# Kernel tuning notes

Hardware: AMD Instinct MI355X
Metric: run time of the kernel (lower is better)

## Reference

```python
import jax, jax.numpy as jnp
import numpy as np

T, B, D, H = 256, 256, 512, 1024


def setup_inputs() -> dict:
    key = jax.random.key(0)
    ks = jax.random.split(key, 9)
    s = 0.02  # small init scale for numerical sanity
    return {
        "inputs": jax.random.normal(ks[0], (T, B, D), dtype=jnp.float32),
        "Wf": jax.random.normal(ks[1], (D + H, H), dtype=jnp.float32) * s,
        "bf": jax.random.normal(ks[2], (H,), dtype=jnp.float32) * s,
        "Wi": jax.random.normal(ks[3], (D + H, H), dtype=jnp.float32) * s,
        "bi": jax.random.normal(ks[4], (H,), dtype=jnp.float32) * s,
        "Wg": jax.random.normal(ks[5], (D + H, H), dtype=jnp.float32) * s,
        "bg": jax.random.normal(ks[6], (H,), dtype=jnp.float32) * s,
        "Wo": jax.random.normal(ks[7], (D + H, H), dtype=jnp.float32) * s,
        "bo": jax.random.normal(ks[8], (H,), dtype=jnp.float32) * s,
    }


def reference(inputs, Wf, bf, Wi, bi, Wg, bg, Wo, bo):
    hidden_dim = Wf.shape[1]
    batch = inputs.shape[1]
    # Fuse the four gate projections into one [D+H, 4H] GEMM per step.
    W = jnp.concatenate([Wf, Wi, Wg, Wo], axis=1)   # [D+H, 4H]
    b = jnp.concatenate([bf, bi, bg, bo], axis=0)   # [4H]

    h0 = jnp.zeros((batch, hidden_dim), dtype=inputs.dtype)
    c0 = jnp.zeros((batch, hidden_dim), dtype=inputs.dtype)

    def step(carry, x):
        hx, cx = carry
        combined = jnp.concatenate([x, hx], axis=1)  # [B, D+H]
        z = combined @ W + b                          # [B, 4H]
        f, i, g, o = jnp.split(z, 4, axis=1)
        f = jax.nn.sigmoid(f)
        i = jax.nn.sigmoid(i)
        g = jnp.tanh(g)
        o = jax.nn.sigmoid(o)
        cx = f * cx + i * g
        hx = o * jnp.tanh(cx)
        return (hx, cx), hx

    (hx, cx), outputs = jax.lax.scan(step, (h0, c0), inputs)
    return outputs, hx, cx
```

## Files before the change

### kernel.cpp

```cpp
#include <hip/hip_runtime.h>
#include <cstdint>
#include <cstddef>

#define T_STEPS 256
#define BATCH   256
#define DIN     512
#define HID     1024
#define KTOT    1536
#define NOUT    4096
#define BHSZ    ((size_t)BATCH * HID)

typedef __bf16 bf16;
typedef __bf16 bf16x4 __attribute__((ext_vector_type(4)));
typedef __bf16 bf16x8 __attribute__((ext_vector_type(8)));
typedef float  f32x4  __attribute__((ext_vector_type(4)));

__device__ __forceinline__ void store_bf16_sc(bf16* p, bf16 v) {
  unsigned short u = __builtin_bit_cast(unsigned short, v);
  asm volatile("global_store_short %0, %1, off sc0 sc1" :: "v"(p), "v"(u) : "memory");
}

#define VMW_(N) asm volatile("s_waitcnt vmcnt(" #N ")" ::: "memory")
#define VMW(N) do { VMW_(N); __builtin_amdgcn_sched_barrier(0); } while (0)
#define LGKM0() do { asm volatile("s_waitcnt lgkmcnt(0)" ::: "memory"); \
                     __builtin_amdgcn_sched_barrier(0); } while (0)
#define SBAR() __builtin_amdgcn_sched_barrier(0)
#define RAWBAR() do { SBAR(); __builtin_amdgcn_s_barrier(); SBAR(); } while (0)

__device__ __forceinline__ float fexp2(float x) {
  float r; asm("v_exp_f32 %0, %1" : "=v"(r) : "v"(x)); return r;
}
__device__ __forceinline__ float frcp(float x) {
  float r; asm("v_rcp_f32 %0, %1" : "=v"(r) : "v"(x)); return r;
}
__device__ __forceinline__ float fsigmoid(float x) {
  return frcp(1.f + fexp2(-1.44269504f * x));
}
__device__ __forceinline__ float ftanh(float x) {
  return 1.f - 2.f * frcp(1.f + fexp2(2.88539008f * x));
}

__global__ void convert_w_kernel(const float* __restrict__ Wf, const float* __restrict__ Wi,
                                 const float* __restrict__ Wg, const float* __restrict__ Wo,
                                 bf16* __restrict__ Wt) {
  __shared__ float tile[64][17];
  const int k0 = blockIdx.x * 64;
  const int jb = blockIdx.y;
  const int j0 = jb * 16;
  const int t  = threadIdx.x;
  const float* srcs[4] = {Wf, Wi, Wg, Wo};
#pragma unroll
  for (int g = 0; g < 4; ++g) {
    const float* src = srcs[g];
    {
      const int jl = t & 15, kb = t >> 4;
#pragma unroll
      for (int r = 0; r < 4; ++r) {
        const int kl = kb + 16 * r;
        tile[kl][jl] = src[(size_t)(k0 + kl) * HID + (j0 + jl)];
      }
    }
    __syncthreads();
    {
      const int kk = t & 63, jl4 = t >> 6;
#pragma unroll
      for (int r = 0; r < 4; ++r) {
        const int jl = jl4 + 4 * r;
        Wt[(size_t)(jb * 64 + g * 16 + jl) * KTOT + (k0 + kk)] = (bf16)tile[kk][jl];
      }
    }
    __syncthreads();
  }
}

__global__ void convert_x_kernel(const float* __restrict__ X, bf16* __restrict__ xb) {
  const int t = blockIdx.y;
  const int i = blockIdx.x * blockDim.x + threadIdx.x;
  const float4 v = ((const float4*)(X + (size_t)t * BATCH * DIN))[i];
  bf16x4 o;
  o[0] = (bf16)v.x; o[1] = (bf16)v.y; o[2] = (bf16)v.z; o[3] = (bf16)v.w;
  ((bf16x4*)(xb + (size_t)t * BATCH * DIN))[i] = o;
}

__global__ __launch_bounds__(512, 2)
void lstm_v14(const bf16* __restrict__ Bt,
              const bf16* __restrict__ xb,
              bf16* __restrict__ hseq,
              const bf16* __restrict__ zb16,
              float* __restrict__ outF,
              const float* __restrict__ bf_, const float* __restrict__ bi_,
              const float* __restrict__ bg_, const float* __restrict__ bo_,
              unsigned* __restrict__ flags) {
  __shared__ f32x4 redu[8][8][64];

  const int tid = threadIdx.x, lane = tid & 63, wid = tid >> 6;
  const int bid = blockIdx.x;
  const int e8  = bid & 7;
  const int mh   = e8 >> 1;
  const int nblk = ((bid >> 3) << 1) | (e8 & 1);
  const int bn0 = nblk * 64;
  const int fr = lane & 15, fq = lane >> 4;
  const int rowA = mh * 32, rowB = 128 + mh * 32;

  if (tid == 0)
    (void)__hip_atomic_load(flags, __ATOMIC_ACQUIRE, __HIP_MEMORY_SCOPE_AGENT);
  __syncthreads();

  const int j = nblk * 16 + fr;
  const float bfv = bf_[j], biv = bi_[j], bgv = bg_[j], bov = bo_[j];
  float crA = 0.f, crB = 0.f;

  bf16x8 breg[6][4];
#pragma unroll
  for (int s = 0; s < 6; ++s) {
    const int ks = wid + 8 * s;
#pragma unroll
    for (int nf = 0; nf < 4; ++nf)
      breg[s][nf] = *(const bf16x8*)(Bt + (size_t)(bn0 + nf * 16 + fr) * KTOT
                                     + ks * 32 + fq * 8);
  }

  bf16x8 P0[2], P1[2], P2[2], P3[2], Q2[2], Q3[2], Q4[2], Q5[2];

  auto ldx = [&](int t2, int rowbase, int s, bf16x8 (&sl)[2]) {
    const bf16* src = xb + (size_t)t2 * BATCH * DIN + (wid + 8 * s) * 32 + fq * 8;
#pragma unroll
    for (int mf = 0; mf < 2; ++mf)
      sl[mf] = *(const bf16x8*)(src + (size_t)(rowbase + mf * 16 + fr) * DIN);
  };
  auto ldh = [&](int t2, int half, int s, bf16x8 (&sl)[2]) {
    const int c0 = (wid + 8 * s) * 32 - 512;
    const int pp = (c0 >> 4) + (fq >> 1);
    const bf16* base = (t2 == 0)
        ? zb16
        : hseq + ((((size_t)(t2 - 1) * 2 + half) << 8) + mh * 64 + pp) * 512;
    const int coloff = (fq & 1) * 8;
#pragma unroll
    for (int mf = 0; mf < 2; ++mf)
      sl[mf] = *(const bf16x8*)(base + (mf * 16 + fr) * 16 + coloff);
  };

  const int pn8 = 2 * wid + ((lane & 7) >> 1) * 16 + (lane & 1);
  auto pollh = [&](int tprev, int half) {
    const unsigned* f = flags + (((size_t)tprev * 2 + half) << 8) + mh * 64 + pn8;
    const unsigned long long tt0 = __builtin_amdgcn_s_memrealtime();
    for (;;) {
      unsigned v = __hip_atomic_load(f, __ATOMIC_RELAXED,
                                     __HIP_MEMORY_SCOPE_AGENT);
      if (__all(v != 0)) break;
      __builtin_amdgcn_s_sleep(1);
      if (__builtin_amdgcn_s_memrealtime() - tt0 > (1ULL << 22)) break;
    }
    asm volatile("" ::: "memory");
    __builtin_amdgcn_sched_barrier(0);
  };

  auto dump = [&](f32x4 (&acc)[2][4]) {
#pragma unroll
    for (int mf = 0; mf < 2; ++mf)
#pragma unroll
      for (int nf = 0; nf < 4; ++nf)
        redu[wid][mf * 4 + nf][lane] = acc[mf][nf];
  };

  auto finish = [&](int t2, int half, float& cre) {
    const int mf_c = wid >> 2;
    const int lsel = (wid & 3) * 16 + fr;
    float z[4];
#pragma unroll
    for (int nf = 0; nf < 4; ++nf) {
      float s_ = 0.f;
#pragma unroll
      for (int s = 0; s < 8; ++s)
        s_ += ((const float*)&redu[s][mf_c * 4 + nf][lsel])[fq];
      z[nf] = s_;
    }
    const float fg = fsigmoid(z[0] + bfv);
    const float ig = fsigmoid(z[1] + biv);
    const float gg = ftanh(z[2] + bgv);
    const float og = fsigmoid(z[3] + bov);
    cre = fg * cre + ig * gg;
    const float h = og * ftanh(cre);
    bf16* tile = hseq + ((((size_t)t2 * 2 + half) << 8) + mh * 64 + nblk) * 512;
    store_bf16_sc(&tile[wid * 64 + lane], (bf16)h);
    const int rowg = half * 128 + mh * 32 + wid * 4 + fq;
    outF[(size_t)t2 * BHSZ + (size_t)rowg * HID + j] = h;
    if (t2 == T_STEPS - 1)
      outF[(size_t)(T_STEPS + 1) * BHSZ + (size_t)rowg * HID + j] = cre;
  };

  auto setflag = [&](int t2, int half) {
    __hip_atomic_store(&flags[(((size_t)t2 * 2 + half) << 8) + mh * 64 + nblk],
                       1u, __ATOMIC_RELAXED, __HIP_MEMORY_SCOPE_AGENT);
  };

#define MFMA8(ACC, SL, S) do {                                              \
    __builtin_amdgcn_s_setprio(1);                                          \
    _Pragma("unroll")                                                       \
    for (int mf_ = 0; mf_ < 2; ++mf_) {                                     \
      _Pragma("unroll")                                                     \
      for (int nf_ = 0; nf_ < 4; ++nf_)                                     \
        ACC[mf_][nf_] = __builtin_amdgcn_mfma_f32_16x16x32_bf16(            \
            SL[mf_], breg[S][nf_], ACC[mf_][nf_], 0, 0, 0);                 \
    }                                                                       \
    __builtin_amdgcn_s_setprio(0);                                          \
  } while (0)

#define STEP(T0, X0, X1, X2, X3, H2, H3, H4, H5) do {                       \
    const int t_ = (T0);                                                    \
    f32x4 accA[2][4] = {}, accB[2][4] = {};                                 \
    VMW(4);                                                                 \
    MFMA8(accA, X0, 0); MFMA8(accA, X1, 1);                                 \
    if (t_ > 0) pollh(t_ - 1, 0);                                           \
    ldh(t_, 0, 2, H2); ldh(t_, 0, 3, H3);                                   \
    ldh(t_, 0, 4, H4); ldh(t_, 0, 5, H5); SBAR();                           \
    VMW(8);                                                                 \
    MFMA8(accB, X2, 0); MFMA8(accB, X3, 1);                                 \
    if (t_ > 0) pollh(t_ - 1, 1);                                           \
    ldh(t_, 1, 2, X0); ldh(t_, 1, 3, X1);                                   \
    ldh(t_, 1, 4, X2); ldh(t_, 1, 5, X3); SBAR();                           \
    VMW(14); MFMA8(accA, H2, 2);                                            \
    VMW(12); MFMA8(accA, H3, 3);                                            \
    VMW(10); MFMA8(accA, H4, 4);                                            \
    VMW(8);  MFMA8(accA, H5, 5);                                            \
    dump(accA); LGKM0(); RAWBAR();                                          \
    finish(t_, 0, crA);                                                     \
    if (t_ + 1 < T_STEPS) {                                                 \
      ldx(t_ + 1, rowA, 0, H2); ldx(t_ + 1, rowA, 1, H3); SBAR();           \
      VMW(6);                            \
    } else {                                                                \
      VMW(3);                                 \
    }                                                                       \
    RAWBAR();                   \
    MFMA8(accB, X0, 2); MFMA8(accB, X1, 3);                                 \
    MFMA8(accB, X2, 4); MFMA8(accB, X3, 5);                                 \
    dump(accB); LGKM0(); RAWBAR();                                          \
    finish(t_, 1, crB);                                                     \
    if (t_ + 1 < T_STEPS) {                                                 \
      ldx(t_ + 1, rowB, 0, H4); ldx(t_ + 1, rowB, 1, H5); SBAR();           \
      VMW(6);                 \
      if (tid == 0) setflag(t_, 0);                                         \
      VMW(4);                                                 \
      if (tid == 0) setflag(t_, 1);                                         \
    } else {                                                                \
      VMW(3);                                \
      if (tid == 0) setflag(t_, 0);                                         \
      VMW(0);                                                               \
      if (tid == 0) setflag(t_, 1);                                         \
    }                                                                       \
    RAWBAR();                     \
  } while (0)

  ldx(0, rowA, 0, P0); SBAR(); ldx(0, rowA, 1, P1); SBAR();
  ldx(0, rowB, 0, P2); SBAR(); ldx(0, rowB, 1, P3); SBAR();
  VMW(4);

#pragma unroll 1
  for (int t = 0; t < T_STEPS; t += 2) {
    STEP(t,     P0, P1, P2, P3, Q2, Q3, Q4, Q5);
    STEP(t + 1, Q2, Q3, Q4, Q5, P0, P1, P2, P3);
  }
#undef STEP
#undef MFMA8
}

__global__ __launch_bounds__(512, 2)
void lstm_fb(const bf16* __restrict__ Bt,
             const float* __restrict__ X,
             const float* __restrict__ zbF,
             float* __restrict__ outF,
             const float* __restrict__ bf_, const float* __restrict__ bi_,
             const float* __restrict__ bg_, const float* __restrict__ bo_,
             unsigned* __restrict__ flags) {
  __shared__ f32x4 redu[8][16][64];
  const int tid = threadIdx.x, lane = tid & 63, wid = tid >> 6;
  const int bid = blockIdx.x;
  const int xcd = bid & 7, sl = bid >> 3;
  const int nblk = xcd * 8 + (sl & 7);
  const int mblk = sl >> 3;
  const int bm0 = mblk * 64;
  const int bn0 = nblk * 64;
  const int fr = lane & 15, fq = lane >> 4;

  if (tid == 0)
    (void)__hip_atomic_load(flags, __ATOMIC_ACQUIRE, __HIP_MEMORY_SCOPE_AGENT);
  __syncthreads();

  const int j = nblk * 16 + fr;
  const float bfv = bf_[j], biv = bi_[j], bgv = bg_[j], bov = bo_[j];
  float cr[2] = {0.f, 0.f};

  bf16x8 breg[6][4];
#pragma unroll
  for (int s = 0; s < 6; ++s) {
    const int ks = wid + 8 * s;
#pragma unroll
    for (int nf = 0; nf < 4; ++nf)
      breg[s][nf] = *(const bf16x8*)(Bt + (size_t)(bn0 + nf * 16 + fr) * KTOT
                                     + ks * 32 + fq * 8);
  }

  bf16x8 afp[2][4];

  auto poll = [&](int tprev) {
    const unsigned* f = flags + (size_t)tprev * 256 + mblk * 64;
    const unsigned long long tt0 = __builtin_amdgcn_s_memrealtime();
    for (;;) {
      unsigned v = __hip_atomic_load(f + lane, __ATOMIC_RELAXED,
                                     __HIP_MEMORY_SCOPE_AGENT);
      if (__all(v != 0)) break;
      __builtin_amdgcn_s_sleep(2);
      if (__builtin_amdgcn_s_memrealtime() - tt0 > (1ULL << 22)) break;
    }
    asm volatile("" ::: "memory");
    __builtin_amdgcn_sched_barrier(0);
  };

  auto loadA = [&](int t2, int s, int p) __attribute__((always_inline)) {
    const int ks = wid + 8 * s;
    const int k = ks * 32 + fq * 8;
    if (s == 2 && t2 > 0) poll(t2 - 1);
    const float* src; int ld, kk;
    if (s < 2) { src = X + (size_t)t2 * BATCH * DIN; ld = DIN; kk = k; }
    else {
      src = (t2 == 0) ? zbF : outF + (size_t)(t2 - 1) * BHSZ;
      ld = HID; kk = k - 512;
    }
#pragma unroll
    for (int mf = 0; mf < 4; ++mf) {
      const float* q = src + (size_t)(bm0 + mf * 16 + fr) * ld + kk;
      const f32x4 lo = *(const f32x4*)q;
      const f32x4 hi = *(const f32x4*)(q + 4);
      bf16x8 v;
      v[0] = (bf16)lo[0]; v[1] = (bf16)lo[1]; v[2] = (bf16)lo[2]; v[3] = (bf16)lo[3];
      v[4] = (bf16)hi[0]; v[5] = (bf16)hi[1]; v[6] = (bf16)hi[2]; v[7] = (bf16)hi[3];
      afp[p][mf] = v;
    }
  };

  loadA(0, 0, 0);

#pragma unroll 1
  for (int t = 0; t < T_STEPS; ++t) {
    f32x4 acc[4][4] = {};
#pragma unroll
    for (int s = 0; s < 6; ++s) {
      if (s < 5)                loadA(t, s + 1, (s + 1) & 1);
      else if (t + 1 < T_STEPS) loadA(t + 1, 0, 0);
      __builtin_amdgcn_s_setprio(1);
#pragma unroll
      for (int mf = 0; mf < 4; ++mf)
#pragma unroll
        for (int nf = 0; nf < 4; ++nf)
          acc[mf][nf] = __builtin_amdgcn_mfma_f32_16x16x32_bf16(
              afp[s & 1][mf], breg[s][nf], acc[mf][nf], 0, 0, 0);
      __builtin_amdgcn_s_setprio(0);
    }

#pragma unroll
    for (int mf = 0; mf < 4; ++mf)
#pragma unroll
      for (int nf = 0; nf < 4; ++nf)
        redu[wid][mf * 4 + nf][lane] = acc[mf][nf];
    __syncthreads();

    const int fbase = (wid >> 1) * 4;
    const int rh = wid & 1;
    float z[2][4];
#pragma unroll
    for (int e = 0; e < 2; ++e) {
      const int rloc = rh * 8 + fq * 2 + e;
      const int lsel = (rloc >> 2) * 16 + fr;
      const int rc = rloc & 3;
#pragma unroll
      for (int nf = 0; nf < 4; ++nf) {
        float sum = 0.f;
#pragma unroll
        for (int s = 0; s < 8; ++s)
          sum += ((const float*)&redu[s][fbase + nf][lsel])[rc];
        z[e][nf] = sum;
      }
    }

    float* outSl = outF + (size_t)t * BHSZ;
#pragma unroll
    for (int e = 0; e < 2; ++e) {
      const float fg = 1.f / (1.f + expf(-(z[e][0] + bfv)));
      const float ig = 1.f / (1.f + expf(-(z[e][1] + biv)));
      const float gg = tanhf(z[e][2] + bgv);
      const float og = 1.f / (1.f + expf(-(z[e][3] + bov)));
      cr[e] = fg * cr[e] + ig * gg;
      const float h = og * tanhf(cr[e]);
      const int m = bm0 + wid * 8 + fq * 2 + e;
      const size_t off = (size_t)m * HID + j;
      __hip_atomic_store(&outSl[off], h, __ATOMIC_RELAXED,
                         __HIP_MEMORY_SCOPE_AGENT);
      if (t == T_STEPS - 1)
        outF[(size_t)(T_STEPS + 1) * BHSZ + off] = cr[e];
    }
    asm volatile("s_waitcnt vmcnt(0)" ::: "memory");
    __syncthreads();
    if (tid == 0)
      __hip_atomic_store(&flags[(size_t)t * 256 + mblk * 64 + nblk], 1u,
                         __ATOMIC_RELAXED, __HIP_MEMORY_SCOPE_AGENT);
  }
}

extern "C" void kernel_launch(void* const* d_in, const int* in_sizes, int n_in,
                              void* d_out, int out_size, void* d_ws, size_t ws_size,
                              hipStream_t stream) {
  const float* X   = (const float*)d_in[0];
  const float* Wf  = (const float*)d_in[1];
  const float* bf_ = (const float*)d_in[2];
  const float* Wi  = (const float*)d_in[3];
  const float* bi_ = (const float*)d_in[4];
  const float* Wg  = (const float*)d_in[5];
  const float* bg_ = (const float*)d_in[6];
  const float* Wo  = (const float*)d_in[7];
  const float* bo_ = (const float*)d_in[8];
  float* out = (float*)d_out;

  const size_t WtB   = (size_t)NOUT * KTOT * 2;
  const size_t zBb   = BHSZ * 4;
  const size_t flagB = (size_t)T_STEPS * 2 * 256 * 4;
  const size_t XbB   = (size_t)T_STEPS * BATCH * DIN * 2;
  const size_t HsB   = (size_t)T_STEPS * 2 * 256 * 1024;

  char* ws = (char*)d_ws;
  bf16*     Wt    = (bf16*)ws;              ws += WtB;
  float*    zbF   = (float*)(void*)ws;      ws += zBb;
  unsigned* flags = (unsigned*)(void*)ws;   ws += flagB;

  const bool big = ws_size >= WtB + zBb + flagB + XbB + HsB + (1u << 20);
  bf16* xbp = nullptr;  bf16* hseq = nullptr;
  if (big) {
    xbp  = (bf16*)ws;   ws += XbB;
    hseq = (bf16*)ws;
  }

  hipMemsetAsync(zbF, 0, zBb + flagB, stream);

  convert_w_kernel<<<dim3(KTOT / 64, NOUT / 64), 256, 0, stream>>>(Wf, Wi, Wg, Wo, Wt);

  if (big) {
    convert_x_kernel<<<dim3(BATCH * DIN / 4 / 256, T_STEPS), 256, 0, stream>>>(X, xbp);
    lstm_v14<<<256, 512, 0, stream>>>(Wt, xbp, hseq, (const bf16*)zbF, out,
                                      bf_, bi_, bg_, bo_, flags);
  } else {
    lstm_fb<<<256, 512, 0, stream>>>(Wt, X, zbF, out,
                                     bf_, bi_, bg_, bo_, flags);
  }

  hipMemcpyAsync(out + (size_t)T_STEPS * BHSZ, out + (size_t)(T_STEPS - 1) * BHSZ,
                 BHSZ * 4, hipMemcpyDeviceToDevice, stream);
}
```

Measured before the change: 2.162 ms.

## Precompute next step's input-projection MFMAs while waiting on recurrent hidden state

Software-pipelines the LSTM step loop so the x-part of the gate GEMM for step t+1 runs during step t, while the kernel waits for the other blocks' hidden state. It does this with double-buffered accumulators and by prefetching x two steps ahead. The goal is to take the input-projection MFMAs off the serial recurrence critical path. In exchange it holds twice as many accumulator registers, which may hurt occupancy or cause spills, and the vmcnt wait counts need careful retuning.

```diff
diff --git a/kernel.cpp b/kernel.cpp
--- a/kernel.cpp
+++ b/kernel.cpp
@@ -83,7 +83,7 @@
 }
 
 __global__ __launch_bounds__(512, 2)
-void lstm_v14(const bf16* __restrict__ Bt,
+void lstm_v15(const bf16* __restrict__ Bt,
               const bf16* __restrict__ xb,
               bf16* __restrict__ hseq,
               const bf16* __restrict__ zb16,
@@ -120,7 +120,8 @@
                                      + ks * 32 + fq * 8);
   }
 
-  bf16x8 P0[2], P1[2], P2[2], P3[2], Q2[2], Q3[2], Q4[2], Q5[2];
+  bf16x8 X0[2], X1[2], X2[2], X3[2], H2[2], H3[2], H4[2], H5[2];
+  f32x4 aA0[2][4], aB0[2][4], aA1[2][4], aB1[2][4];
 
   auto ldx = [&](int t2, int rowbase, int s, bf16x8 (&sl)[2]) {
     const bf16* src = xb + (size_t)t2 * BATCH * DIN + (wid + 8 * s) * 32 + fq * 8;
@@ -206,44 +207,58 @@
     __builtin_amdgcn_s_setprio(0);                                          \
   } while (0)
 
-#define STEP(T0, X0, X1, X2, X3, H2, H3, H4, H5) do {                       \
+#define ZERO8(ACC) do {                                                     \
+    _Pragma("unroll")                                                       \
+    for (int mf_ = 0; mf_ < 2; ++mf_) {                                     \
+      _Pragma("unroll")                                                     \
+      for (int nf_ = 0; nf_ < 4; ++nf_)                                     \
+        ACC[mf_][nf_] = (f32x4){0.f, 0.f, 0.f, 0.f};                        \
+    }                                                                       \
+  } while (0)
+
+#define STEP(T0, CA, CB, NA, NB) do {                                       \
     const int t_ = (T0);                                                    \
-    f32x4 accA[2][4] = {}, accB[2][4] = {};                                 \
-    VMW(4);                                                                 \
-    MFMA8(accA, X0, 0); MFMA8(accA, X1, 1);                                 \
+    const bool hasNext = (t_ + 1 < T_STEPS);                                \
+    const bool hasNext2 = (t_ + 2 < T_STEPS);                               \
+    if (hasNext) { ZERO8(NA); ZERO8(NB); }                                  \
     if (t_ > 0) pollh(t_ - 1, 0);                                           \
     ldh(t_, 0, 2, H2); ldh(t_, 0, 3, H3);                                   \
     ldh(t_, 0, 4, H4); ldh(t_, 0, 5, H5); SBAR();                           \
-    VMW(8);                                                                 \
-    MFMA8(accB, X2, 0); MFMA8(accB, X3, 1);                                 \
+    if (hasNext) {                                                          \
+      VMW(12); MFMA8(NA, X0, 0); MFMA8(NA, X1, 1);       \
+      VMW(8);  MFMA8(NB, X2, 0); MFMA8(NB, X3, 1);       \
+    }                                                                       \
     if (t_ > 0) pollh(t_ - 1, 1);                                           \
     ldh(t_, 1, 2, X0); ldh(t_, 1, 3, X1);                                   \
     ldh(t_, 1, 4, X2); ldh(t_, 1, 5, X3); SBAR();                           \
-    VMW(14); MFMA8(accA, H2, 2);                                            \
-    VMW(12); MFMA8(accA, H3, 3);                                            \
-    VMW(10); MFMA8(accA, H4, 4);                                            \
-    VMW(8);  MFMA8(accA, H5, 5);                                            \
-    dump(accA); LGKM0(); RAWBAR();                                          \
-    finish(t_, 0, crA);                                                     \
-    if (t_ + 1 < T_STEPS) {                                                 \
-      ldx(t_ + 1, rowA, 0, H2); ldx(t_ + 1, rowA, 1, H3); SBAR();           \
-      VMW(6);                            \
-    } else {                                                                \
-      VMW(3);                                 \
-    }                                                                       \
+    VMW(14); MFMA8(CA, H2, 2);                                              \
+    VMW(12); MFMA8(CA, H3, 3);                                              \
+    VMW(10); MFMA8(CA, H4, 4);                                              \
+    VMW(8);  MFMA8(CA, H5, 5);                                              \
+    dump(CA); LGKM0(); RAWBAR();                                            \
+    finish(t_, 0, crA);                                     \
+    VMW(8);                                               \
     RAWBAR();                   \
-    MFMA8(accB, X0, 2); MFMA8(accB, X1, 3);                                 \
-    MFMA8(accB, X2, 4); MFMA8(accB, X3, 5);                                 \
-    dump(accB); LGKM0(); RAWBAR();                                          \
-    finish(t_, 1, crB);                                                     \
-    if (t_ + 1 < T_STEPS) {                                                 \
-      ldx(t_ + 1, rowB, 0, H4); ldx(t_ + 1, rowB, 1, H5); SBAR();           \
-      VMW(6);                 \
+    MFMA8(CB, X0, 2);                                                       \
+    VMW(6); MFMA8(CB, X1, 3);                                               \
+    VMW(4); MFMA8(CB, X2, 4);                                               \
+    VMW(2); MFMA8(CB, X3, 5);                                               \
+    dump(CB); LGKM0(); RAWBAR();                                            \
+    finish(t_, 1, crB);                                     \
+    if (hasNext2) {                                                         \
+      ldx(t_ + 2, rowA, 0, X0); ldx(t_ + 2, rowA, 1, X1);                   \
+      ldx(t_ + 2, rowB, 0, X2); ldx(t_ + 2, rowB, 1, X3); SBAR();           \
+      VMW(10);                        \
       if (tid == 0) setflag(t_, 0);                                         \
-      VMW(4);                                                 \
+      VMW(8);                           \
+      if (tid == 0) setflag(t_, 1);                                         \
+    } else if (t_ == T_STEPS - 1) {                                         \
+      VMW(3);                     \
+      if (tid == 0) setflag(t_, 0);                                         \
+      VMW(0);                                                               \
       if (tid == 0) setflag(t_, 1);                                         \
     } else {                                                                \
-      VMW(3);                                \
+      VMW(2);                        \
       if (tid == 0) setflag(t_, 0);                                         \
       VMW(0);                                                               \
       if (tid == 0) setflag(t_, 1);                                         \
@@ -251,16 +266,21 @@
     RAWBAR();                     \
   } while (0)
 
-  ldx(0, rowA, 0, P0); SBAR(); ldx(0, rowA, 1, P1); SBAR();
-  ldx(0, rowB, 0, P2); SBAR(); ldx(0, rowB, 1, P3); SBAR();
-  VMW(4);
+  ldx(0, rowA, 0, X0); SBAR(); ldx(0, rowA, 1, X1); SBAR();
+  ldx(0, rowB, 0, X2); SBAR(); ldx(0, rowB, 1, X3); SBAR();
+  ZERO8(aA0); ZERO8(aB0);
+  VMW(4); MFMA8(aA0, X0, 0); MFMA8(aA0, X1, 1);
+  VMW(0); MFMA8(aB0, X2, 0); MFMA8(aB0, X3, 1);
+  ldx(1, rowA, 0, X0); SBAR(); ldx(1, rowA, 1, X1); SBAR();
+  ldx(1, rowB, 0, X2); SBAR(); ldx(1, rowB, 1, X3); SBAR();
 
 #pragma unroll 1
   for (int t = 0; t < T_STEPS; t += 2) {
-    STEP(t,     P0, P1, P2, P3, Q2, Q3, Q4, Q5);
-    STEP(t + 1, Q2, Q3, Q4, Q5, P0, P1, P2, P3);
+    STEP(t,     aA0, aB0, aA1, aB1);
+    STEP(t + 1, aA1, aB1, aA0, aB0);
   }
 #undef STEP
+#undef ZERO8
 #undef MFMA8
 }
 
@@ -444,7 +464,7 @@
 
   if (big) {
     convert_x_kernel<<<dim3(BATCH * DIN / 4 / 256, T_STEPS), 256, 0, stream>>>(X, xbp);
-    lstm_v14<<<256, 512, 0, stream>>>(Wt, xbp, hseq, (const bf16*)zbF, out,
+    lstm_v15<<<256, 512, 0, stream>>>(Wt, xbp, hseq, (const bf16*)zbF, out,
                                       bf_, bi_, bg_, bo_, flags);
   } else {
     lstm_fb<<<256, 512, 0, stream>>>(Wt, X, zbF, out,
```

Result: slower. 4.660 ms (+115.6%).
